# Optimization experiments

Hardware: AMD Instinct MI355X
Metric: run time of the kernel (lower is better)

Reference implementation:

```python
import jax, jax.numpy as jnp
import numpy as np

FIXED_POINT = 4
LOGMAX = 7
MAX_INT8 = 127
B, H = 16384, 2048


def _clipped_add(*ts):
    r = ts[0].astype(jnp.int32)
    for t in ts[1:]:
        r = r + t.astype(jnp.int32)
    return jnp.clip(r, -MAX_INT8, MAX_INT8).astype(jnp.int8)


def _int_matmul(x, w):
    # x: (..., in) int8, w: (out, in) int8 -> (..., out) int8
    r = jnp.matmul(x.astype(jnp.int32), w.T.astype(jnp.int32))
    scale = (2 ** FIXED_POINT) * int(np.sqrt(w.shape[-1]))  # 16 * 45 = 720 for H=2048
    r = r // scale  # floor division, matches torch // on ints
    return jnp.clip(r, -MAX_INT8, MAX_INT8).astype(jnp.int8)


def setup_inputs() -> dict:
    key = jax.random.key(0)
    k_x, k_s, k_wf, k_uf, k_wh, k_uh = jax.random.split(key, 6)

    def init_w(k):
        w = jax.random.normal(k, (H, H), dtype=jnp.float32) * (2 ** FIXED_POINT)
        return jnp.clip(jnp.round(w), -MAX_INT8, MAX_INT8).astype(jnp.int8)

    x = jax.random.randint(k_x, (B, H), -MAX_INT8, MAX_INT8 + 1, dtype=jnp.int32).astype(jnp.int8)
    state = jax.random.randint(k_s, (B, H), -MAX_INT8, MAX_INT8 + 1, dtype=jnp.int32).astype(jnp.int8)
    return {
        "x": x,
        "state": state,
        "W_f": init_w(k_wf),
        "U_f": init_w(k_uf),
        "b_f": jnp.zeros((H,), dtype=jnp.int8),
        "W_h": init_w(k_wh),
        "U_h": init_w(k_uh),
        "b_h": jnp.zeros((H,), dtype=jnp.int8),
    }


def reference(x, state, W_f, U_f, b_f, W_h, U_h, b_h):
    f_t = _clipped_add(_int_matmul(x, W_f), _int_matmul(state, U_f), b_f)
    f_gate = f_t.astype(jnp.int32) + MAX_INT8  # in [0, 254]
    # note: torch `a >> LOGMAX + 1` parses as a >> (LOGMAX + 1) == >> 8 (arithmetic shift)
    gated_past = (f_gate * state.astype(jnp.int32)) >> (LOGMAX + 1)
    gated_past = jnp.clip(gated_past, -MAX_INT8, MAX_INT8).astype(jnp.int8)
    h_tilde = _clipped_add(_int_matmul(x, W_h), _int_matmul(gated_past, U_h), b_h)
    diff = h_tilde.astype(jnp.int32) - state.astype(jnp.int32)
    new_state = state.astype(jnp.int32) + ((f_gate * diff) >> (LOGMAX + 1))
    new_state = jnp.clip(new_state, -MAX_INT8, MAX_INT8).astype(jnp.int8)
    return (new_state, new_state)
```

## Files before the change

### kernel.cpp

```cpp
#include <hip/hip_runtime.h>
#include <stdint.h>

#define HH 2048
#define BB 16384
#define NK (HH / 64)

typedef int v4i __attribute__((ext_vector_type(4)));

__device__ __forceinline__ int clip127(int v){
  v = v > 127 ? 127 : v;
  return v < -127 ? -127 : v;
}
__device__ __forceinline__ int fdiv720(int r){
  int q = r / 720;
  return q - ((r - q * 720) < 0 ? 1 : 0);
}

__global__ void pack_i32_to_i8(const int* __restrict__ src, int8_t* __restrict__ dst, int n16){
  int stride = gridDim.x * blockDim.x;
  for (int i = blockIdx.x * blockDim.x + threadIdx.x; i < n16; i += stride){
    const int4* s = (const int4*)src + (size_t)i * 4;
    int4 a = s[0], b = s[1], c = s[2], d = s[3];
    int4 o;
    o.x = (a.x & 255) | ((a.y & 255) << 8) | ((a.z & 255) << 16) | (a.w << 24);
    o.y = (b.x & 255) | ((b.y & 255) << 8) | ((b.z & 255) << 16) | (b.w << 24);
    o.z = (c.x & 255) | ((c.y & 255) << 8) | ((c.z & 255) << 16) | (c.w << 24);
    o.w = (d.x & 255) | ((d.y & 255) << 8) | ((d.z & 255) << 16) | (d.w << 24);
    ((int4*)dst)[i] = o;
  }
}

__global__ void dup_out(const int* __restrict__ src, int* __restrict__ dst, int n4){
  int stride = gridDim.x * blockDim.x;
  for (int i = blockIdx.x * blockDim.x + threadIdx.x; i < n4; i += stride)
    ((int4*)dst)[i] = ((const int4*)src)[i];
}

template<int PHASE>
__global__ __launch_bounds__(256, 2)
void gemm_dual(const int8_t* __restrict__ A1, const int8_t* __restrict__ A2,
               const int8_t* __restrict__ B1, const int8_t* __restrict__ B2,
               const int* __restrict__ bias,
               const int8_t* __restrict__ state8,
               int* fbuf, int8_t* __restrict__ g8out, int* __restrict__ out2)
{
  __shared__ __align__(16) int8_t lds[2 * 32768];
  const int tid  = threadIdx.x;
  const int lane = tid & 63;
  const int wave = tid >> 6;
  const int wrow = wave >> 1, wcol = wave & 1;

  const int bid = blockIdx.x;
  const int wg  = (bid & 7) * 256 + (bid >> 3);
  const int rowbase = (wg >> 4) * 128;
  const int colbase = (wg & 15) * 128;

  v4i accA[4][4], accB[4][4];
  const v4i vzero = {0, 0, 0, 0};
#pragma unroll
  for (int m = 0; m < 4; m++)
#pragma unroll
    for (int n = 0; n < 4; n++){ accA[m][n] = vzero; accB[m][n] = vzero; }

  const int srow   = tid >> 2;
  const int schunk = tid & 3;
  const int chunk  = lane >> 4;
  const int rl     = lane & 15;

  auto STAGE = [&](int buf, int kk){
    const int k0 = kk * 64;
    const int bb = buf * 32768;
#pragma unroll
    for (int p = 0; p < 2; p++){
      const int row = p * 64 + srow;
      const int swc = schunk ^ ((row >> 1) & 3);
      const size_t aoff = (size_t)(rowbase + row) * HH + k0 + swc * 16;
      const size_t boff = (size_t)(colbase + row) * HH + k0 + swc * 16;
      const int ldst = bb + p * 4096 + tid * 16;
      __builtin_amdgcn_global_load_lds((const __attribute__((address_space(1))) void*)(A1 + aoff),
                                       (__attribute__((address_space(3))) void*)(lds + ldst), 16, 0, 0);
      __builtin_amdgcn_global_load_lds((const __attribute__((address_space(1))) void*)(A2 + aoff),
                                       (__attribute__((address_space(3))) void*)(lds + 8192 + ldst), 16, 0, 0);
      __builtin_amdgcn_global_load_lds((const __attribute__((address_space(1))) void*)(B1 + boff),
                                       (__attribute__((address_space(3))) void*)(lds + 16384 + ldst), 16, 0, 0);
      __builtin_amdgcn_global_load_lds((const __attribute__((address_space(1))) void*)(B2 + boff),
                                       (__attribute__((address_space(3))) void*)(lds + 24576 + ldst), 16, 0, 0);
    }
  };

  STAGE(0, 0);
  asm volatile("s_waitcnt vmcnt(0)" ::: "memory");
  __builtin_amdgcn_s_barrier();

  int cur = 0;
  for (int kk = 0; kk < NK; ++kk){
    __builtin_amdgcn_sched_barrier(0);
    if (kk + 1 < NK) STAGE(cur ^ 1, kk + 1);
    const int cb = cur * 32768;
    {
      v4i af[4], bf[4];
#pragma unroll
      for (int m = 0; m < 4; m++){
        const int row = wrow * 64 + m * 16 + rl;
        af[m] = *(const v4i*)(lds + cb + row * 64 + ((chunk ^ ((row >> 1) & 3)) << 4));
      }
#pragma unroll
      for (int n = 0; n < 4; n++){
        const int row = wcol * 64 + n * 16 + rl;
        bf[n] = *(const v4i*)(lds + cb + 16384 + row * 64 + ((chunk ^ ((row >> 1) & 3)) << 4));
      }
#pragma unroll
      for (int m = 0; m < 4; m++)
#pragma unroll
        for (int n = 0; n < 4; n++)
          accA[m][n] = __builtin_amdgcn_mfma_i32_16x16x64_i8(af[m], bf[n], accA[m][n], 0, 0, 0);
    }
    {
      v4i af[4], bf[4];
#pragma unroll
      for (int m = 0; m < 4; m++){
        const int row = wrow * 64 + m * 16 + rl;
        af[m] = *(const v4i*)(lds + cb + 8192 + row * 64 + ((chunk ^ ((row >> 1) & 3)) << 4));
      }
#pragma unroll
      for (int n = 0; n < 4; n++){
        const int row = wcol * 64 + n * 16 + rl;
        bf[n] = *(const v4i*)(lds + cb + 24576 + row * 64 + ((chunk ^ ((row >> 1) & 3)) << 4));
      }
#pragma unroll
      for (int m = 0; m < 4; m++)
#pragma unroll
        for (int n = 0; n < 4; n++)
          accB[m][n] = __builtin_amdgcn_mfma_i32_16x16x64_i8(af[m], bf[n], accB[m][n], 0, 0, 0);
    }
    __builtin_amdgcn_sched_barrier(0);
    asm volatile("s_waitcnt vmcnt(0)" ::: "memory");
    __builtin_amdgcn_s_barrier();
    cur ^= 1;
  }

  const int q = lane >> 4;
#pragma unroll
  for (int m = 0; m < 4; m++){
#pragma unroll
    for (int n = 0; n < 4; n++){
      const int gcol = colbase + wcol * 64 + n * 16 + rl;
      const int bval = bias[gcol];
#pragma unroll
      for (int r = 0; r < 4; r++){
        const int grow = rowbase + wrow * 64 + m * 16 + q * 4 + r;
        const size_t idx = (size_t)grow * HH + gcol;
        const int v1 = clip127(fdiv720(accA[m][n][r]));
        const int v2 = clip127(fdiv720(accB[m][n][r]));
        const int t  = clip127(v1 + v2 + bval);
        const int st = state8[idx];
        if (PHASE == 1){
          const int fg = t + 127;
          fbuf[idx]  = fg;
          g8out[idx] = (int8_t)clip127((fg * st) >> 8);
        } else {
          const int fg = fbuf[idx];
          const int ns = clip127(st + ((fg * (t - st)) >> 8));
          fbuf[idx] = ns;
          if (out2) out2[idx] = ns;
        }
      }
    }
  }
}

extern "C" void kernel_launch(void* const* d_in, const int* in_sizes, int n_in,
                              void* d_out, int out_size, void* d_ws, size_t ws_size,
                              hipStream_t stream){
  const int* x  = (const int*)d_in[0];
  const int* st = (const int*)d_in[1];
  const int* Wf = (const int*)d_in[2];
  const int* Uf = (const int*)d_in[3];
  const int* bf = (const int*)d_in[4];
  const int* Wh = (const int*)d_in[5];
  const int* Uh = (const int*)d_in[6];
  const int* bh = (const int*)d_in[7];

  const size_t NBH = (size_t)BB * HH;
  const size_t NW  = (size_t)HH * HH;
  const size_t need = 3 * NBH + 4 * NW;

  int*    out1   = (int*)d_out;
  const bool wsp = (ws_size >= need);
  int8_t* base   = wsp ? (int8_t*)d_ws : (int8_t*)d_out + NBH * 4;
  int8_t* x8  = base;
  int8_t* s8  = x8 + NBH;
  int8_t* g8  = s8 + NBH;
  int8_t* wf8 = g8 + NBH;
  int8_t* uf8 = wf8 + NW;
  int8_t* wh8 = uf8 + NW;
  int8_t* uh8 = wh8 + NW;

  pack_i32_to_i8<<<2048, 256, 0, stream>>>(x,  x8,  (int)(NBH / 16));
  pack_i32_to_i8<<<2048, 256, 0, stream>>>(st, s8,  (int)(NBH / 16));
  pack_i32_to_i8<<<1024, 256, 0, stream>>>(Wf, wf8, (int)(NW / 16));
  pack_i32_to_i8<<<1024, 256, 0, stream>>>(Uf, uf8, (int)(NW / 16));
  pack_i32_to_i8<<<1024, 256, 0, stream>>>(Wh, wh8, (int)(NW / 16));
  pack_i32_to_i8<<<1024, 256, 0, stream>>>(Uh, uh8, (int)(NW / 16));

  gemm_dual<1><<<2048, 256, 0, stream>>>(x8, s8, wf8, uf8, bf, s8, out1, g8, nullptr);
  gemm_dual<2><<<2048, 256, 0, stream>>>(x8, g8, wh8, uh8, bh, s8, out1, nullptr,
                                         wsp ? out1 + NBH : nullptr);

  if (!wsp)
    dup_out<<<2048, 256, 0, stream>>>(out1, out1 + NBH, (int)(NBH / 4));
}
```

Baseline: 622.2 us.

## Deepen GEMM prefetch pipeline, remap tile grid, and fuse pack kernels

The six int32-to-int8 pack launches are merged into one grid-stride kernel, which removes launch overhead and tail effects. In the dual GEMM, the K-loop now issues two stages ahead and waits on vmcnt(8) instead of draining all loads, so global-to-LDS traffic for step k+1 overlaps compute on step k. The workgroup-to-tile mapping also changes so that groups of consecutive blocks share the same row panel and adjacent column tiles. The cost is an extra barrier per iteration, and the new mapping may reuse the L2 cache differently.

New measurement: 623.7 us. No clear change (+0.2%).

```diff
diff --git a/kernel.cpp b/kernel.cpp
--- a/kernel.cpp
+++ b/kernel.cpp
@@ -4,6 +4,8 @@
 #define HH 2048
 #define BB 16384
 #define NK (HH / 64)
+#define NBH16 (1 << 21)
+#define NW16  (1 << 18)
 
 typedef int v4i __attribute__((ext_vector_type(4)));
 
@@ -16,17 +18,36 @@
   return q - ((r - q * 720) < 0 ? 1 : 0);
 }
 
-__global__ void pack_i32_to_i8(const int* __restrict__ src, int8_t* __restrict__ dst, int n16){
-  int stride = gridDim.x * blockDim.x;
-  for (int i = blockIdx.x * blockDim.x + threadIdx.x; i < n16; i += stride){
-    const int4* s = (const int4*)src + (size_t)i * 4;
-    int4 a = s[0], b = s[1], c = s[2], d = s[3];
-    int4 o;
-    o.x = (a.x & 255) | ((a.y & 255) << 8) | ((a.z & 255) << 16) | (a.w << 24);
-    o.y = (b.x & 255) | ((b.y & 255) << 8) | ((b.z & 255) << 16) | (b.w << 24);
-    o.z = (c.x & 255) | ((c.y & 255) << 8) | ((c.z & 255) << 16) | (c.w << 24);
-    o.w = (d.x & 255) | ((d.y & 255) << 8) | ((d.z & 255) << 16) | (d.w << 24);
-    ((int4*)dst)[i] = o;
+__device__ __forceinline__ void pack16(const int* __restrict__ src, int8_t* __restrict__ dst, int i){
+  const int4* s = (const int4*)src + (size_t)i * 4;
+  int4 a = s[0], b = s[1], c = s[2], d = s[3];
+  int4 o;
+  o.x = (a.x & 255) | ((a.y & 255) << 8) | ((a.z & 255) << 16) | (a.w << 24);
+  o.y = (b.x & 255) | ((b.y & 255) << 8) | ((b.z & 255) << 16) | (b.w << 24);
+  o.z = (c.x & 255) | ((c.y & 255) << 8) | ((c.z & 255) << 16) | (c.w << 24);
+  o.w = (d.x & 255) | ((d.y & 255) << 8) | ((d.z & 255) << 16) | (d.w << 24);
+  ((int4*)dst)[i] = o;
+}
+
+__global__ void pack_all(const int* __restrict__ x,  const int* __restrict__ st,
+                         const int* __restrict__ Wf, const int* __restrict__ Uf,
+                         const int* __restrict__ Wh, const int* __restrict__ Uh,
+                         int8_t* x8, int8_t* s8, int8_t* wf8, int8_t* uf8,
+                         int8_t* wh8, int8_t* uh8){
+  const int total = 2 * NBH16 + 4 * NW16;
+  const int stride = gridDim.x * blockDim.x;
+  for (int u = blockIdx.x * blockDim.x + threadIdx.x; u < total; u += stride){
+    if (u < NBH16)            pack16(x,  x8,  u);
+    else if (u < 2 * NBH16)   pack16(st, s8,  u - NBH16);
+    else {
+      const int v = u - 2 * NBH16;
+      const int w = v >> 18;
+      const int i = v & (NW16 - 1);
+      if      (w == 0) pack16(Wf, wf8, i);
+      else if (w == 1) pack16(Uf, uf8, i);
+      else if (w == 2) pack16(Wh, wh8, i);
+      else             pack16(Uh, uh8, i);
+    }
   }
 }
 
@@ -51,9 +72,9 @@
   const int wrow = wave >> 1, wcol = wave & 1;
 
   const int bid = blockIdx.x;
-  const int wg  = (bid & 7) * 256 + (bid >> 3);
-  const int rowbase = (wg >> 4) * 128;
-  const int colbase = (wg & 15) * 128;
+  const int j   = bid >> 3;
+  const int rowbase = (j >> 1) * 128;
+  const int colbase = ((bid & 7) * 2 + (j & 1)) * 128;
 
   v4i accA[4][4], accB[4][4];
   const v4i vzero = {0, 0, 0, 0};
@@ -88,15 +109,7 @@
     }
   };
 
-  STAGE(0, 0);
-  asm volatile("s_waitcnt vmcnt(0)" ::: "memory");
-  __builtin_amdgcn_s_barrier();
-
-  int cur = 0;
-  for (int kk = 0; kk < NK; ++kk){
-    __builtin_amdgcn_sched_barrier(0);
-    if (kk + 1 < NK) STAGE(cur ^ 1, kk + 1);
-    const int cb = cur * 32768;
+  auto COMPUTE = [&](int cb){
     {
       v4i af[4], bf[4];
 #pragma unroll
@@ -133,11 +146,24 @@
         for (int n = 0; n < 4; n++)
           accB[m][n] = __builtin_amdgcn_mfma_i32_16x16x64_i8(af[m], bf[n], accB[m][n], 0, 0, 0);
     }
+  };
+
+  STAGE(0, 0);
+  STAGE(1, 1);
+
+  for (int kk = 0; kk < NK - 1; ++kk){
     __builtin_amdgcn_sched_barrier(0);
-    asm volatile("s_waitcnt vmcnt(0)" ::: "memory");
+    asm volatile("s_waitcnt vmcnt(8)" ::: "memory");
     __builtin_amdgcn_s_barrier();
-    cur ^= 1;
+    COMPUTE((kk & 1) * 32768);
+    __builtin_amdgcn_sched_barrier(0);
+    __builtin_amdgcn_s_barrier();
+    if (kk + 2 < NK) STAGE(kk & 1, kk + 2);
   }
+  __builtin_amdgcn_sched_barrier(0);
+  asm volatile("s_waitcnt vmcnt(0)" ::: "memory");
+  __builtin_amdgcn_s_barrier();
+  COMPUTE(((NK - 1) & 1) * 32768);
 
   const int q = lane >> 4;
 #pragma unroll
@@ -196,12 +222,8 @@
   int8_t* wh8 = uf8 + NW;
   int8_t* uh8 = wh8 + NW;
 
-  pack_i32_to_i8<<<2048, 256, 0, stream>>>(x,  x8,  (int)(NBH / 16));
-  pack_i32_to_i8<<<2048, 256, 0, stream>>>(st, s8,  (int)(NBH / 16));
-  pack_i32_to_i8<<<1024, 256, 0, stream>>>(Wf, wf8, (int)(NW / 16));
-  pack_i32_to_i8<<<1024, 256, 0, stream>>>(Uf, uf8, (int)(NW / 16));
-  pack_i32_to_i8<<<1024, 256, 0, stream>>>(Wh, wh8, (int)(NW / 16));
-  pack_i32_to_i8<<<1024, 256, 0, stream>>>(Uh, uh8, (int)(NW / 16));
+  pack_all<<<2048, 256, 0, stream>>>(x, st, Wf, Uf, Wh, Uh,
+                                     x8, s8, wf8, uf8, wh8, uh8);
 
   gemm_dual<1><<<2048, 256, 0, stream>>>(x8, s8, wf8, uf8, bf, s8, out1, g8, nullptr);
   gemm_dual<2><<<2048, 256, 0, stream>>>(x8, g8, wh8, uh8, bh, s8, out1, nullptr,
```
